# Kernel optimization log

Measured on AMD Instinct MI355X. Metric: run time of the kernel, lower is better.

## Reference

```python
import jax, jax.numpy as jnp
import numpy as np

OUT, IN, R = 8192, 8192, 16
GROUP = 16
SCALING = 16.0 / 16.0  # lora_alpha / r
# nvfp4 (e2m1) code table: 3 low bits magnitude, bit 3 = sign
NVFP4_LUT = jnp.array([0.0, 0.5, 1.0, 1.5, 2.0, 3.0, 4.0, 6.0,
                       -0.0, -0.5, -1.0, -1.5, -2.0, -3.0, -4.0, -6.0],
                      dtype=jnp.float32)


def setup_inputs() -> dict:
    key = jax.random.key(0)
    k1, k2, k3, k4, k5 = jax.random.split(key, 5)
    x = jax.random.normal(k1, (64, IN), dtype=jnp.float32)
    packed_weight = jax.random.randint(k2, (OUT, IN // 2), 0, 256, dtype=jnp.int32).astype(jnp.uint8)
    # effective block scales (global scale already absorbed, as in _load_prequantized_nvfp4)
    weight_block_scales = (jax.random.uniform(k3, (OUT, IN // GROUP), dtype=jnp.float32) + 0.1) * 0.01
    lora_A = jax.random.normal(k4, (R, IN), dtype=jnp.float32) * (1.0 / np.sqrt(IN))
    lora_B = jax.random.normal(k5, (OUT, R), dtype=jnp.float32) * 0.01
    return {"x": x, "packed_weight": packed_weight,
            "weight_block_scales": weight_block_scales,
            "lora_A": lora_A, "lora_B": lora_B}


def _dequant_nvfp4(packed, block_scales):
    # packed: (OUT, IN//2) uint8, two fp4 codes per byte (low nibble = even index)
    low = (packed & 0xF).astype(jnp.int32)
    high = (packed >> 4).astype(jnp.int32)
    codes = jnp.stack([low, high], axis=-1).reshape(packed.shape[0], -1)  # (OUT, IN)
    vals = NVFP4_LUT[codes]
    O, I = vals.shape
    # per-block scale over groups of GROUP along in_features
    W = (vals.reshape(O, I // GROUP, GROUP) * block_scales[:, :, None]).reshape(O, I)
    return W


def reference(x, packed_weight, weight_block_scales, lora_A, lora_B):
    W = _dequant_nvfp4(packed_weight, weight_block_scales)      # (OUT, IN) fp32
    base = x @ W.T                                              # (B, OUT)
    lora = (x @ lora_A.T) @ lora_B.T                            # (B, OUT)
    return base + SCALING * lora
```

## Files before the change

### kernel.cpp

```cpp
#include <hip/hip_runtime.h>
#include <stdint.h>

#define IN_F   8192
#define OUT_F  8192
#define MB     64
#define RANK   16
#define KSPLIT 16
#define NTILE  128

typedef _Float16 f16x8 __attribute__((ext_vector_type(8)));
typedef float    f32x4 __attribute__((ext_vector_type(4)));
typedef unsigned u32x4 __attribute__((ext_vector_type(4)));

__device__ __forceinline__ unsigned pk2h(float a, float b) {
    return __builtin_bit_cast(unsigned, __builtin_amdgcn_cvt_pkrtz(a, b));
}

__device__ __forceinline__ float decode_fp4(unsigned nib, float schalf) {
    unsigned c = nib & 0xFu;
    int hv = (int)((0xC8643210u >> ((c & 7u) * 4u)) & 0xFu);
    int iv = (c & 8u) ? -hv : hv;
    return (float)iv * schalf;
}

__device__ __forceinline__ unsigned dec_byte(unsigned bv, float schalf) {
    return pk2h(decode_fp4(bv, schalf), decode_fp4(bv >> 4, schalf));
}

__global__ void detect_kernel(const unsigned* __restrict__ Wp, int* __restrict__ flag) {
    unsigned v = Wp[threadIdx.x & 63];
    unsigned long long m = __ballot(v > 255u);
    if (threadIdx.x == 0) *flag = (m == 0ull) ? 1 : 0;
}

__global__ __launch_bounds__(256) void prep_kernel(
    const float* __restrict__ x, const float* __restrict__ lora_A,
    const float* __restrict__ lora_B,
    uint2* __restrict__ xf2, float* __restrict__ out)
{
    const int m = blockIdx.x;
    const int tid = threadIdx.x;
    const int mt = m >> 4, l15 = m & 15;
    float acc[RANK];
#pragma unroll
    for (int r = 0; r < RANK; ++r) acc[r] = 0.f;

    const float4* x4 = (const float4*)(x + (size_t)m * IN_F);
    const float4* A4 = (const float4*)lora_A;
    for (int j = tid; j < IN_F / 4; j += 256) {
        float4 xv = x4[j];
        uint2 u;
        u.x = pk2h(xv.x, xv.y);
        u.y = pk2h(xv.z, xv.w);
        int kstep = j >> 3, quad = (j >> 1) & 3, h = j & 1;
        xf2[(size_t)(((kstep * 4 + mt) * 64 + quad * 16 + l15) * 2 + h)] = u;
#pragma unroll
        for (int r = 0; r < RANK; ++r) {
            float4 av = A4[(size_t)r * (IN_F / 4) + j];
            acc[r] += xv.x * av.x + xv.y * av.y + xv.z * av.z + xv.w * av.w;
        }
    }
#pragma unroll
    for (int r = 0; r < RANK; ++r)
#pragma unroll
        for (int off = 32; off > 0; off >>= 1)
            acc[r] += __shfl_down(acc[r], off);

    __shared__ float red[4][RANK];
    __shared__ __align__(16) float tsh[RANK];
    int lane = tid & 63, wid = tid >> 6;
    if (lane == 0) {
#pragma unroll
        for (int r = 0; r < RANK; ++r) red[wid][r] = acc[r];
    }
    __syncthreads();
    if (tid < RANK)
        tsh[tid] = red[0][tid] + red[1][tid] + red[2][tid] + red[3][tid];
    __syncthreads();

    float4 ta = *(const float4*)&tsh[0];
    float4 tb = *(const float4*)&tsh[4];
    float4 tc = *(const float4*)&tsh[8];
    float4 td = *(const float4*)&tsh[12];
    float* orow = out + (size_t)m * OUT_F;
#pragma unroll 4
    for (int j = 0; j < OUT_F / 256; ++j) {
        int n = j * 256 + tid;
        const float4* B4 = (const float4*)(lora_B + (size_t)n * RANK);
        float4 b0 = B4[0], b1 = B4[1], b2 = B4[2], b3 = B4[3];
        orow[n] = ta.x * b0.x + ta.y * b0.y + ta.z * b0.z + ta.w * b0.w
                + tb.x * b1.x + tb.y * b1.y + tb.z * b1.z + tb.w * b1.w
                + tc.x * b2.x + tc.y * b2.y + tc.z * b2.z + tc.w * b2.w
                + td.x * b3.x + td.y * b3.y + td.z * b3.z + td.w * b3.w;
    }
}

template<int FMT>
__global__ __launch_bounds__(256) void main_kernel(
    const void*  __restrict__ Wpv,
    const float* __restrict__ scales,
    const uint4* __restrict__ xf4,
    const int*   __restrict__ flag,
    float*       __restrict__ out)
{
    if (*flag != FMT) return;

    const int ks  = blockIdx.x;
    const int nb  = blockIdx.y;
    const int tid = threadIdx.x;
    const int lane = tid & 63, w = tid >> 6;
    const int l15 = lane & 15, quad = lane >> 4;

    const int kbase   = ks * (IN_F / KSPLIT);
    const int kbase32 = kbase >> 5;
    const int n0 = nb * NTILE + w * 32;

    f32x4 acc[4][2];
#pragma unroll
    for (int mt = 0; mt < 4; ++mt)
#pragma unroll
        for (int nt = 0; nt < 2; ++nt)
            acc[mt][nt] = (f32x4){0.f, 0.f, 0.f, 0.f};

    const int4*    wi0 = (const int4*)Wpv + (size_t)(n0 + l15) * (IN_F / 2 / 4);
    const int4*    wi1 = wi0 + (size_t)16 * (IN_F / 2 / 4);
    const uint8_t* wb0 = (const uint8_t*)Wpv + (size_t)(n0 + l15) * (IN_F / 2);
    const uint8_t* wb1 = wb0 + (size_t)16 * (IN_F / 2);
    const float*   sp0 = scales + (size_t)(n0 + l15) * (IN_F / 16);
    const float*   sp1 = sp0 + (size_t)16 * (IN_F / 16);

#pragma unroll 4
    for (int s = 0; s < (IN_F / KSPLIT) / 32; ++s) {
        const int kstep = kbase32 + s;
        f16x8 afr[4];
#pragma unroll
        for (int mt = 0; mt < 4; ++mt)
            afr[mt] = __builtin_bit_cast(f16x8, xf4[(size_t)(kstep * 4 + mt) * 64 + lane]);

        const int kk = kbase + s * 32 + quad * 8;
#pragma unroll
        for (int nt = 0; nt < 2; ++nt) {
            const float* sp = nt ? sp1 : sp0;
            float schalf = 0.5f * sp[kk >> 4];
            unsigned by0, by1, by2, by3;
            if (FMT == 1) {
                const int4* wi = nt ? wi1 : wi0;
                int4 v = wi[kk >> 3];
                by0 = (unsigned)v.x; by1 = (unsigned)v.y;
                by2 = (unsigned)v.z; by3 = (unsigned)v.w;
            } else {
                const uint8_t* wb = nt ? wb1 : wb0;
                unsigned w32 = *(const unsigned*)(wb + (kk >> 1));
                by0 = w32 & 0xFFu; by1 = (w32 >> 8) & 0xFFu;
                by2 = (w32 >> 16) & 0xFFu; by3 = w32 >> 24;
            }
            u32x4 bu;
            bu[0] = dec_byte(by0, schalf);
            bu[1] = dec_byte(by1, schalf);
            bu[2] = dec_byte(by2, schalf);
            bu[3] = dec_byte(by3, schalf);
            f16x8 b = __builtin_bit_cast(f16x8, bu);
#pragma unroll
            for (int mt = 0; mt < 4; ++mt)
                acc[mt][nt] = __builtin_amdgcn_mfma_f32_16x16x32_f16(
                    afr[mt], b, acc[mt][nt], 0, 0, 0);
        }
    }

#pragma unroll
    for (int mt = 0; mt < 4; ++mt)
#pragma unroll
        for (int nt = 0; nt < 2; ++nt)
#pragma unroll
            for (int r = 0; r < 4; ++r) {
                int m = mt * 16 + quad * 4 + r;
                int n = n0 + nt * 16 + l15;
                atomicAdd(&out[(size_t)m * OUT_F + n], acc[mt][nt][r]);
            }
}

extern "C" void kernel_launch(void* const* d_in, const int* in_sizes, int n_in,
                              void* d_out, int out_size, void* d_ws, size_t ws_size,
                              hipStream_t stream)
{
    (void)in_sizes; (void)n_in; (void)out_size; (void)ws_size;
    const float* x      = (const float*)d_in[0];
    const void*  Wp     = (const void*)d_in[1];
    const float* scales = (const float*)d_in[2];
    const float* lora_A = (const float*)d_in[3];
    const float* lora_B = (const float*)d_in[4];
    float* out = (float*)d_out;

    char* ws = (char*)d_ws;
    int*   flag = (int*)ws;
    uint2* xf   = (uint2*)(ws + 4096);

    detect_kernel<<<1, 64, 0, stream>>>((const unsigned*)Wp, flag);
    prep_kernel<<<64, 256, 0, stream>>>(x, lora_A, lora_B, xf, out);
    main_kernel<1><<<dim3(KSPLIT, OUT_F / NTILE), 256, 0, stream>>>(
        Wp, scales, (const uint4*)xf, flag, out);
    main_kernel<0><<<dim3(KSPLIT, OUT_F / NTILE), 256, 0, stream>>>(
        Wp, scales, (const uint4*)xf, flag, out);
}
```

Baseline: 276.9 us.

## Restructure GEMV into per-row-tile blocks with LDS K-reduction and perm-based fp4 decode

```diff
diff --git a/kernel.cpp b/kernel.cpp
--- a/kernel.cpp
+++ b/kernel.cpp
@@ -5,40 +5,49 @@
 #define OUT_F  8192
 #define MB     64
 #define RANK   16
-#define KSPLIT 16
-#define NTILE  128
 
 typedef _Float16 f16x8 __attribute__((ext_vector_type(8)));
+typedef _Float16 f16x2 __attribute__((ext_vector_type(2)));
 typedef float    f32x4 __attribute__((ext_vector_type(4)));
-typedef unsigned u32x4 __attribute__((ext_vector_type(4)));
 
 __device__ __forceinline__ unsigned pk2h(float a, float b) {
     return __builtin_bit_cast(unsigned, __builtin_amdgcn_cvt_pkrtz(a, b));
 }
 
-__device__ __forceinline__ float decode_fp4(unsigned nib, float schalf) {
-    unsigned c = nib & 0xFu;
-    int hv = (int)((0xC8643210u >> ((c & 7u) * 4u)) & 0xFu);
-    int iv = (c & 8u) ? -hv : hv;
-    return (float)iv * schalf;
-}
-
-__device__ __forceinline__ unsigned dec_byte(unsigned bv, float schalf) {
-    return pk2h(decode_fp4(bv, schalf), decode_fp4(bv >> 4, schalf));
-}
-
-__global__ void detect_kernel(const unsigned* __restrict__ Wp, int* __restrict__ flag) {
+__device__ __forceinline__ f16x8 decode8(unsigned p, unsigned s2) {
+    unsigned q  = p >> 4;
+    unsigned me = __builtin_amdgcn_perm(0x46444240u, 0x3E3C3800u, p & 0x07070707u);
+    unsigned mo = __builtin_amdgcn_perm(0x46444240u, 0x3E3C3800u, q & 0x07070707u);
+    unsigned he = ((p & 0x08080808u) << 4) | me;
+    unsigned ho = ((q & 0x08080808u) << 4) | mo;
+    unsigned bu0 = __builtin_amdgcn_perm(ho, he, 0x040C000Cu);
+    unsigned bu1 = __builtin_amdgcn_perm(ho, he, 0x050C010Cu);
+    unsigned bu2 = __builtin_amdgcn_perm(ho, he, 0x060C020Cu);
+    unsigned bu3 = __builtin_amdgcn_perm(ho, he, 0x070C030Cu);
+    f16x2 sv = __builtin_bit_cast(f16x2, s2);
+    f16x2 h0 = __builtin_bit_cast(f16x2, bu0) * sv;
+    f16x2 h1 = __builtin_bit_cast(f16x2, bu1) * sv;
+    f16x2 h2 = __builtin_bit_cast(f16x2, bu2) * sv;
+    f16x2 h3 = __builtin_bit_cast(f16x2, bu3) * sv;
+    f16x8 b;
+    b[0]=h0[0]; b[1]=h0[1]; b[2]=h1[0]; b[3]=h1[1];
+    b[4]=h2[0]; b[5]=h2[1]; b[6]=h3[0]; b[7]=h3[1];
+    return b;
+}
+
+__global__ void detect_kernel(const unsigned* __restrict__ Wp,
+                              int* __restrict__ flag, float* __restrict__ t) {
     unsigned v = Wp[threadIdx.x & 63];
     unsigned long long m = __ballot(v > 255u);
     if (threadIdx.x == 0) *flag = (m == 0ull) ? 1 : 0;
+    for (int i = threadIdx.x; i < MB * RANK; i += 256) t[i] = 0.f;
 }
 
 __global__ __launch_bounds__(256) void prep_kernel(
     const float* __restrict__ x, const float* __restrict__ lora_A,
-    const float* __restrict__ lora_B,
-    uint2* __restrict__ xf2, float* __restrict__ out)
-{
-    const int m = blockIdx.x;
+    uint2* __restrict__ xf2, float* __restrict__ t)
+{
+    const int m = blockIdx.x, kq = blockIdx.y;
     const int tid = threadIdx.x;
     const int mt = m >> 4, l15 = m & 15;
     float acc[RANK];
@@ -47,7 +56,9 @@
 
     const float4* x4 = (const float4*)(x + (size_t)m * IN_F);
     const float4* A4 = (const float4*)lora_A;
-    for (int j = tid; j < IN_F / 4; j += 256) {
+#pragma unroll
+    for (int it = 0; it < 2; ++it) {
+        int j = kq * 512 + it * 256 + tid;
         float4 xv = x4[j];
         uint2 u;
         u.x = pk2h(xv.x, xv.y);
@@ -67,7 +78,6 @@
             acc[r] += __shfl_down(acc[r], off);
 
     __shared__ float red[4][RANK];
-    __shared__ __align__(16) float tsh[RANK];
     int lane = tid & 63, wid = tid >> 6;
     if (lane == 0) {
 #pragma unroll
@@ -75,28 +85,35 @@
     }
     __syncthreads();
     if (tid < RANK)
-        tsh[tid] = red[0][tid] + red[1][tid] + red[2][tid] + red[3][tid];
-    __syncthreads();
-
-    float4 ta = *(const float4*)&tsh[0];
-    float4 tb = *(const float4*)&tsh[4];
-    float4 tc = *(const float4*)&tsh[8];
-    float4 td = *(const float4*)&tsh[12];
-    float* orow = out + (size_t)m * OUT_F;
-#pragma unroll 4
-    for (int j = 0; j < OUT_F / 256; ++j) {
-        int n = j * 256 + tid;
-        const float4* B4 = (const float4*)(lora_B + (size_t)n * RANK);
+        atomicAdd(&t[m * RANK + tid],
+                  red[0][tid] + red[1][tid] + red[2][tid] + red[3][tid]);
+}
+
+__global__ __launch_bounds__(256) void lora_kernel(
+    const float* __restrict__ t, const float* __restrict__ lora_B,
+    float* __restrict__ out)
+{
+    const int gid = blockIdx.x * 256 + threadIdx.x;
+    const int m = gid >> 11;
+    const int n4 = (gid & 2047) * 4;
+    const float4* t4 = (const float4*)(t + m * RANK);
+    float4 ta = t4[0], tb = t4[1], tc = t4[2], td = t4[3];
+    float4 o;
+    float* op = (float*)&o;
+#pragma unroll
+    for (int j = 0; j < 4; ++j) {
+        const float4* B4 = (const float4*)(lora_B + (size_t)(n4 + j) * RANK);
         float4 b0 = B4[0], b1 = B4[1], b2 = B4[2], b3 = B4[3];
-        orow[n] = ta.x * b0.x + ta.y * b0.y + ta.z * b0.z + ta.w * b0.w
-                + tb.x * b1.x + tb.y * b1.y + tb.z * b1.z + tb.w * b1.w
-                + tc.x * b2.x + tc.y * b2.y + tc.z * b2.z + tc.w * b2.w
-                + td.x * b3.x + td.y * b3.y + td.z * b3.z + td.w * b3.w;
-    }
+        op[j] = ta.x * b0.x + ta.y * b0.y + ta.z * b0.z + ta.w * b0.w
+              + tb.x * b1.x + tb.y * b1.y + tb.z * b1.z + tb.w * b1.w
+              + tc.x * b2.x + tc.y * b2.y + tc.z * b2.z + tc.w * b2.w
+              + td.x * b3.x + td.y * b3.y + td.z * b3.z + td.w * b3.w;
+    }
+    ((float4*)out)[gid] = o;
 }
 
 template<int FMT>
-__global__ __launch_bounds__(256) void main_kernel(
+__global__ __launch_bounds__(1024, 4) void main_kernel(
     const void*  __restrict__ Wpv,
     const float* __restrict__ scales,
     const uint4* __restrict__ xf4,
@@ -105,78 +122,59 @@
 {
     if (*flag != FMT) return;
 
-    const int ks  = blockIdx.x;
-    const int nb  = blockIdx.y;
+    __shared__ float lds[16 * 1024];
+
     const int tid = threadIdx.x;
     const int lane = tid & 63, w = tid >> 6;
     const int l15 = lane & 15, quad = lane >> 4;
-
-    const int kbase   = ks * (IN_F / KSPLIT);
-    const int kbase32 = kbase >> 5;
-    const int n0 = nb * NTILE + w * 32;
-
-    f32x4 acc[4][2];
-#pragma unroll
-    for (int mt = 0; mt < 4; ++mt)
-#pragma unroll
-        for (int nt = 0; nt < 2; ++nt)
-            acc[mt][nt] = (f32x4){0.f, 0.f, 0.f, 0.f};
-
-    const int4*    wi0 = (const int4*)Wpv + (size_t)(n0 + l15) * (IN_F / 2 / 4);
-    const int4*    wi1 = wi0 + (size_t)16 * (IN_F / 2 / 4);
-    const uint8_t* wb0 = (const uint8_t*)Wpv + (size_t)(n0 + l15) * (IN_F / 2);
-    const uint8_t* wb1 = wb0 + (size_t)16 * (IN_F / 2);
-    const float*   sp0 = scales + (size_t)(n0 + l15) * (IN_F / 16);
-    const float*   sp1 = sp0 + (size_t)16 * (IN_F / 16);
+    const int n0 = blockIdx.x * 16;
+    const int row = n0 + l15;
+
+    f32x4 acc[4];
+#pragma unroll
+    for (int mt = 0; mt < 4; ++mt) acc[mt] = (f32x4){0.f, 0.f, 0.f, 0.f};
+
+    const uint4*    wi = (const uint4*)Wpv + (size_t)row * (IN_F / 8) + w * 64 + quad;
+    const unsigned* wb = (const unsigned*)((const uint8_t*)Wpv
+                         + (size_t)row * (IN_F / 2)) + w * 64 + quad;
+    const float*    sp = scales + (size_t)row * (IN_F / 16) + w * 32 + (quad >> 1);
 
 #pragma unroll 4
-    for (int s = 0; s < (IN_F / KSPLIT) / 32; ++s) {
-        const int kstep = kbase32 + s;
+    for (int s = 0; s < 16; ++s) {
+        const int kstep = w * 16 + s;
         f16x8 afr[4];
 #pragma unroll
         for (int mt = 0; mt < 4; ++mt)
             afr[mt] = __builtin_bit_cast(f16x8, xf4[(size_t)(kstep * 4 + mt) * 64 + lane]);
 
-        const int kk = kbase + s * 32 + quad * 8;
-#pragma unroll
-        for (int nt = 0; nt < 2; ++nt) {
-            const float* sp = nt ? sp1 : sp0;
-            float schalf = 0.5f * sp[kk >> 4];
-            unsigned by0, by1, by2, by3;
-            if (FMT == 1) {
-                const int4* wi = nt ? wi1 : wi0;
-                int4 v = wi[kk >> 3];
-                by0 = (unsigned)v.x; by1 = (unsigned)v.y;
-                by2 = (unsigned)v.z; by3 = (unsigned)v.w;
-            } else {
-                const uint8_t* wb = nt ? wb1 : wb0;
-                unsigned w32 = *(const unsigned*)(wb + (kk >> 1));
-                by0 = w32 & 0xFFu; by1 = (w32 >> 8) & 0xFFu;
-                by2 = (w32 >> 16) & 0xFFu; by3 = w32 >> 24;
-            }
-            u32x4 bu;
-            bu[0] = dec_byte(by0, schalf);
-            bu[1] = dec_byte(by1, schalf);
-            bu[2] = dec_byte(by2, schalf);
-            bu[3] = dec_byte(by3, schalf);
-            f16x8 b = __builtin_bit_cast(f16x8, bu);
-#pragma unroll
-            for (int mt = 0; mt < 4; ++mt)
-                acc[mt][nt] = __builtin_amdgcn_mfma_f32_16x16x32_f16(
-                    afr[mt], b, acc[mt][nt], 0, 0, 0);
+        unsigned p;
+        if (FMT == 1) {
+            uint4 v = wi[s * 4];
+            p = v.x | (v.y << 8) | (v.z << 16) | (v.w << 24);
+        } else {
+            p = wb[s * 4];
         }
+        float sc = sp[s * 2];
+        unsigned s2 = pk2h(sc, sc);
+        f16x8 b = decode8(p, s2);
+#pragma unroll
+        for (int mt = 0; mt < 4; ++mt)
+            acc[mt] = __builtin_amdgcn_mfma_f32_16x16x32_f16(afr[mt], b, acc[mt], 0, 0, 0);
     }
 
 #pragma unroll
     for (int mt = 0; mt < 4; ++mt)
 #pragma unroll
-        for (int nt = 0; nt < 2; ++nt)
-#pragma unroll
-            for (int r = 0; r < 4; ++r) {
-                int m = mt * 16 + quad * 4 + r;
-                int n = n0 + nt * 16 + l15;
-                atomicAdd(&out[(size_t)m * OUT_F + n], acc[mt][nt][r]);
-            }
+        for (int r = 0; r < 4; ++r)
+            lds[w * 1024 + (mt * 16 + quad * 4 + r) * 16 + l15] = acc[mt][r];
+    __syncthreads();
+
+    float sum = 0.f;
+#pragma unroll
+    for (int w2 = 0; w2 < 16; ++w2) sum += lds[w2 * 1024 + tid];
+    const int m = tid >> 4, nl = tid & 15;
+    const size_t idx = (size_t)m * OUT_F + n0 + nl;
+    out[idx] += sum;
 }
 
 extern "C" void kernel_launch(void* const* d_in, const int* in_sizes, int n_in,
@@ -193,12 +191,14 @@
 
     char* ws = (char*)d_ws;
     int*   flag = (int*)ws;
-    uint2* xf   = (uint2*)(ws + 4096);
-
-    detect_kernel<<<1, 64, 0, stream>>>((const unsigned*)Wp, flag);
-    prep_kernel<<<64, 256, 0, stream>>>(x, lora_A, lora_B, xf, out);
-    main_kernel<1><<<dim3(KSPLIT, OUT_F / NTILE), 256, 0, stream>>>(
+    float* t    = (float*)(ws + 4096);
+    uint2* xf   = (uint2*)(ws + 65536);
+
+    detect_kernel<<<1, 256, 0, stream>>>((const unsigned*)Wp, flag, t);
+    prep_kernel<<<dim3(64, 4), 256, 0, stream>>>(x, lora_A, xf, t);
+    lora_kernel<<<512, 256, 0, stream>>>(t, lora_B, out);
+    main_kernel<1><<<OUT_F / 16, 1024, 0, stream>>>(
         Wp, scales, (const uint4*)xf, flag, out);
-    main_kernel<0><<<dim3(KSPLIT, OUT_F / NTILE), 256, 0, stream>>>(
+    main_kernel<0><<<OUT_F / 16, 1024, 0, stream>>>(
         Wp, scales, (const uint4*)xf, flag, out);
 }
```

Result: faster. 258.4 us (-6.7%).
